# Kernel optimization log

Hardware: AMD Instinct MI355X
Metric: run time of the kernel (lower is better)

## Reference

```python
import jax, jax.numpy as jnp
import numpy as np

DIM = 3072
NHEADS = 24
HEAD_DIM = DIM // NHEADS  # 128
C = HEAD_DIM // 2         # 64 rotary pairs
B = 2
L = 2048
MAXPOS = 64
EPS = 1e-6
C1 = C - 2 * (C // 3)     # 22 (F band)
C2 = C // 3               # 21 (H band)
C3 = C // 3               # 21 (W band)


def _rope_table():
    # cos/sin table [MAXPOS, C, 2]; three independent frequency bands (F,H,W)
    pos = np.arange(MAXPOS, dtype=np.float32)
    parts = []
    for ck in (C1, C2, C3):
        inv = 1.0 / (10000.0 ** (np.arange(ck, dtype=np.float32) / ck))
        ang = np.outer(pos, inv)
        parts.append(np.stack([np.cos(ang), np.sin(ang)], axis=-1))
    return np.concatenate(parts, axis=1).astype(np.float32)


def setup_inputs() -> dict:
    key = jax.random.key(0)
    ks = jax.random.split(key, 12)
    x = jax.random.normal(ks[0], (B, L, DIM), dtype=jnp.float32)
    grid_sizes = np.array([[4, 16, 28], [4, 16, 32]], dtype=np.int32)  # ragged: 1792, 2048 tokens
    seq_lens = np.array([g[0] * g[1] * g[2] for g in grid_sizes], dtype=np.int32)
    freqs = jnp.asarray(_rope_table())
    w_scale = 0.02
    wq = jax.random.normal(ks[1], (DIM, DIM), dtype=jnp.float32) * w_scale
    wk = jax.random.normal(ks[2], (DIM, DIM), dtype=jnp.float32) * w_scale
    wv = jax.random.normal(ks[3], (DIM, DIM), dtype=jnp.float32) * w_scale
    wo = jax.random.normal(ks[4], (DIM, DIM), dtype=jnp.float32) * w_scale
    bq = jnp.zeros((DIM,), jnp.float32)
    bk = jnp.zeros((DIM,), jnp.float32)
    bv = jnp.zeros((DIM,), jnp.float32)
    bo = jnp.zeros((DIM,), jnp.float32)
    gq = jnp.ones((DIM,), jnp.float32)  # norm_q weight
    gk = jnp.ones((DIM,), jnp.float32)  # norm_k weight
    return {"x": x, "seq_lens": seq_lens, "grid_sizes": grid_sizes, "freqs": freqs,
            "wq": wq, "bq": bq, "wk": wk, "bk": bk, "wv": wv, "bv": bv,
            "wo": wo, "bo": bo, "gq": gq, "gk": gk}


def _rmsnorm(x, g):
    # WanRMSNorm: normalize in bf16, cast back, scale by bf16 weight
    xb = x.astype(jnp.bfloat16)
    n = xb * jax.lax.rsqrt(jnp.mean(xb * xb, axis=-1, keepdims=True) + jnp.bfloat16(EPS))
    return n.astype(x.dtype) * g.astype(jnp.bfloat16)


def _build_rot(grid_sizes, freqs):
    # Per-sample 3D rope rotation table [B, L, C, 2]; padded tail gets identity rotation
    gs = np.asarray(grid_sizes)
    rots = []
    for f, h, w in gs.tolist():
        s = f * h * w
        bf = jnp.broadcast_to(freqs[:f, :C1][:, None, None], (f, h, w, C1, 2))
        bh = jnp.broadcast_to(freqs[:h, C1:C1 + C2][None, :, None], (f, h, w, C2, 2))
        bw = jnp.broadcast_to(freqs[:w, C1 + C2:][None, None, :], (f, h, w, C3, 2))
        rot = jnp.concatenate([bf, bh, bw], axis=3).reshape(s, C, 2)
        if s < L:
            ident = jnp.zeros((L - s, C, 2), freqs.dtype).at[..., 0].set(1.0)
            rot = jnp.concatenate([rot, ident], axis=0)
        rots.append(rot)
    return jnp.stack(rots)


def _apply_rope(x, rot):
    # complex multiply expressed as real rotation; matches rope_apply_3d, output rounded to bf16
    xr = x.reshape(B, L, NHEADS, C, 2)
    cos = rot[:, :, None, :, 0]
    sin = rot[:, :, None, :, 1]
    out_r = xr[..., 0] * cos - xr[..., 1] * sin
    out_i = xr[..., 0] * sin + xr[..., 1] * cos
    out = jnp.stack([out_r, out_i], axis=-1).reshape(B, L, NHEADS, HEAD_DIM)
    return out.astype(jnp.bfloat16).astype(x.dtype)


def reference(x, seq_lens, grid_sizes, freqs, wq, bq, wk, bk, wv, bv, wo, bo, gq, gk):
    q = _rmsnorm(x @ wq + bq, gq).reshape(B, L, NHEADS, HEAD_DIM)
    k = _rmsnorm(x @ wk + bk, gk).reshape(B, L, NHEADS, HEAD_DIM)
    v = (x @ wv + bv).reshape(B, L, NHEADS, HEAD_DIM)
    rot = _build_rot(grid_sizes, freqs)
    q = _apply_rope(q, rot)
    k = _apply_rope(k, rot)
    scale = 1.0 / np.sqrt(HEAD_DIM).astype(np.float32)
    scores = jnp.einsum('bsnd,btnd->bnst', q, k) * scale  # [B, H, L, L]
    kmask = (jnp.arange(L)[None, :] < jnp.asarray(seq_lens)[:, None])[:, None, None, :]
    scores = jnp.where(kmask, scores, jnp.float32(-1e9))
    probs = jax.nn.softmax(scores, axis=-1)
    out = jnp.einsum('bnst,btnd->bsnd', probs, v).reshape(B, L, DIM)
    return out @ wo + bo
```

## Files before the change

### kernel.cpp

```cpp
#include <hip/hip_runtime.h>
#include <stdint.h>
#include <stddef.h>


typedef __attribute__((ext_vector_type(8))) short short8;
typedef __attribute__((ext_vector_type(4))) float f32x4;
typedef __attribute__((ext_vector_type(4))) unsigned short ushort4v;
typedef __attribute__((address_space(1))) uint32_t gu32;
typedef __attribute__((address_space(3))) uint32_t lu32;

__device__ __forceinline__ float btof(unsigned short u){
  union { float f; uint32_t i; } x; x.i = ((uint32_t)u) << 16; return x.f;
}
__device__ __forceinline__ unsigned short ftob(float f){
  uint32_t u = __builtin_bit_cast(uint32_t, f);
  u += 0x7fffu + ((u >> 16) & 1u);
  return (unsigned short)(u >> 16);
}
__device__ __forceinline__ float rb(float f){ return btof(ftob(f)); }

__device__ __forceinline__ void async_cp16(const void* g, void* l){
  __builtin_amdgcn_global_load_lds((gu32*)g, (lu32*)l, 16, 0, 0);
}

__device__ __forceinline__ void barrier_raw(){
  asm volatile("" ::: "memory");
  __builtin_amdgcn_s_barrier();
  asm volatile("" ::: "memory");
}

__device__ __forceinline__ f32x4 vmax4(f32x4 a, f32x4 b){
  f32x4 r;
  r[0] = fmaxf(a[0], b[0]); r[1] = fmaxf(a[1], b[1]);
  r[2] = fmaxf(a[2], b[2]); r[3] = fmaxf(a[3], b[3]);
  return r;
}

#define VMW4 asm volatile("s_waitcnt vmcnt(4)" ::: "memory")
#define VMW2 asm volatile("s_waitcnt vmcnt(2)" ::: "memory")
#define VMW0 asm volatile("s_waitcnt vmcnt(0)" ::: "memory")


__global__ __launch_bounds__(256) void k_convert_x(const float* __restrict__ x,
                                                   unsigned short* __restrict__ xb){
  int i = (blockIdx.x * 256 + threadIdx.x) * 4;
  float4 v = *(const float4*)(x + i);
  ushort4v o = { ftob(v.x), ftob(v.y), ftob(v.z), ftob(v.w) };
  *(ushort4v*)(xb + i) = o;
}

__global__ __launch_bounds__(256) void k_bias(const float* __restrict__ bq,
                                              const float* __restrict__ bk,
                                              const float* __restrict__ bv,
                                              float* __restrict__ bias9){
  int i = blockIdx.x * 256 + threadIdx.x;
  const float* s = (i < 3072) ? bq : ((i < 6144) ? bk : bv);
  bias9[i] = s[i % 3072];
}

__global__ __launch_bounds__(256) void k_wt(const float* __restrict__ wq,
                                            const float* __restrict__ wk,
                                            const float* __restrict__ wv,
                                            const float* __restrict__ wo,
                                            unsigned short* __restrict__ WTqkv,
                                            unsigned short* __restrict__ woT){
  __shared__ float tile[64][65];
  int k0 = blockIdx.x * 64;
  int n0g = blockIdx.y * 64;
  const float* src; unsigned short* dst; int col0, drow0;
  if (n0g < 9216){
    int sel = n0g / 3072;
    src = (sel == 0) ? wq : ((sel == 1) ? wk : wv);
    col0 = n0g % 3072; dst = WTqkv; drow0 = n0g;
  } else { src = wo; col0 = n0g - 9216; dst = woT; drow0 = n0g - 9216; }
  for (int i = 0; i < 16; i++){
    int idx = i * 256 + threadIdx.x;
    int r = idx >> 6, c = idx & 63;
    tile[r][c] = src[(size_t)(k0 + r) * 3072 + col0 + c];
  }
  __syncthreads();
  for (int i = 0; i < 16; i++){
    int idx = i * 256 + threadIdx.x;
    int rr = idx >> 6, cc = idx & 63;
    dst[(size_t)(drow0 + rr) * 3072 + k0 + cc] = ftob(tile[cc][rr]);
  }
}

template <bool OUT_BF16>
__global__ __launch_bounds__(512, 2) void k_gemm(const unsigned short* __restrict__ A,
                                                 const unsigned short* __restrict__ BT,
                                                 const float* __restrict__ bias,
                                                 void* __restrict__ Cout, int N, int K){
  extern __shared__ unsigned short lds[];
  unsigned short* AsL = lds;
  unsigned short* BsL = lds + 32768;

  int tid = threadIdx.x;
  int w = tid >> 6, lane = tid & 63;
  int quad = lane >> 4, l16 = lane & 15;
  int wr = w >> 2, wc = w & 3;
  int m0 = blockIdx.y * 256, n0 = blockIdx.x * 256;

  f32x4 acc[8][4] = {};
  short8 af[4][2], b0[2][2], b1[2][2];

  auto lda = [&](const unsigned short* base, int mh){
#pragma unroll
    for (int im = 0; im < 4; im++)
#pragma unroll
      for (int kk = 0; kk < 2; kk++){
        int j = wr * 64 + mh * 32 + im * 8 + (l16 >> 1);
        int lc = ((l16 & 1) << 3) | (kk << 2) | quad;
        af[im][kk] = *(const short8*)(base + j * 128 + (lc ^ (j & 15)) * 8);
      }
  };
  auto ldb = [&](const unsigned short* base, short8 (&bb)[2][2], int nh){
#pragma unroll
    for (int in = 0; in < 2; in++)
#pragma unroll
      for (int kk = 0; kk < 2; kk++){
        int j = wc * 32 + nh * 16 + in * 8 + (l16 >> 1);
        int lc = ((l16 & 1) << 3) | (kk << 2) | quad;
        bb[in][kk] = *(const short8*)(base + j * 128 + (lc ^ (j & 15)) * 8);
      }
  };
  auto mfmaQ = [&](int mh, short8 (&bb)[2][2], int nh){
    __builtin_amdgcn_s_setprio(1);
#pragma unroll
    for (int im = 0; im < 4; im++)
#pragma unroll
      for (int in = 0; in < 2; in++)
#pragma unroll
        for (int kk = 0; kk < 2; kk++)
          acc[mh * 4 + im][nh * 2 + in] =
            __builtin_amdgcn_mfma_f32_16x16x32_bf16(af[im][kk], bb[in][kk],
                                                    acc[mh * 4 + im][nh * 2 + in], 0, 0, 0);
    __builtin_amdgcn_s_setprio(0);
  };

  auto stageA = [&](unsigned short* dst, int kt, int mh){
#pragma unroll
    for (int i = 0; i < 2; i++){
      int idx0 = (w * 2 + i) * 8;
      int mr0 = (((idx0 >> 6) << 7) | (idx0 & 63)) | (mh << 6);
      int jb = mr0 >> 1;
      int j = jb + (lane >> 4);
      int lc = (lane & 15) ^ (j & 15);
      int mr = (j << 1) + (lc >> 3);
      async_cp16(A + (size_t)(m0 + mr) * K + kt + (lc & 7) * 8, dst + jb * 128);
    }
  };
  auto stageB = [&](unsigned short* dst, int kt, int nh){
#pragma unroll
    for (int i = 0; i < 2; i++){
      int idx0 = (w * 2 + i) * 8;
      int nr0 = (((idx0 >> 5) << 6) | (idx0 & 31)) | (nh << 5);
      int jb = nr0 >> 1;
      int j = jb + (lane >> 4);
      int lc = (lane & 15) ^ (j & 15);
      int nr = (j << 1) + (lc >> 3);
      async_cp16(BT + (size_t)(n0 + nr) * K + kt + (lc & 7) * 8, dst + jb * 128);
    }
  };

  int nt = K >> 6;
  stageA(AsL, 0, 0); stageB(BsL, 0, 0); stageB(BsL, 0, 1); stageA(AsL, 0, 1);
  VMW4; barrier_raw();

  for (int t = 0; t < nt; t++){
    unsigned short* Asb = AsL + (t & 1) * 16384;
    unsigned short* Bsb = BsL + (t & 1) * 16384;
    unsigned short* Asn = AsL + ((t & 1) ^ 1) * 16384;
    unsigned short* Bsn = BsL + ((t & 1) ^ 1) * 16384;
    int ktn = (t + 1) << 6;
    bool more = (t + 1 < nt);

    lda(Asb, 0); ldb(Bsb, b0, 0);
    if (more) stageA(Asn, ktn, 0);
    VMW4; barrier_raw();
    mfmaQ(0, b0, 0);
    barrier_raw();

    ldb(Bsb, b1, 1);
    if (more){ stageB(Bsn, ktn, 0); VMW4; } else VMW2;
    barrier_raw();
    mfmaQ(0, b1, 1);
    barrier_raw();

    lda(Asb, 1);
    if (more){ stageB(Bsn, ktn, 1); VMW4; } else VMW0;
    barrier_raw();
    mfmaQ(1, b1, 1);
    barrier_raw();

    if (more){ stageA(Asn, ktn, 1); VMW4; }
    barrier_raw();
    mfmaQ(1, b0, 0);
    barrier_raw();
  }

#pragma unroll
  for (int img = 0; img < 8; img++){
    int row = m0 + wr * 128 + img * 16 + quad * 4;
#pragma unroll
    for (int ing = 0; ing < 4; ing++){
      int col = n0 + wc * 64 + ing * 16 + l16;
      float bb = bias[col];
      f32x4 v = acc[img][ing];
#pragma unroll
      for (int r = 0; r < 4; r++){
        float out = v[r] + bb;
        if (OUT_BF16) ((unsigned short*)Cout)[(size_t)(row + r) * N + col] = ftob(out);
        else          ((float*)Cout)[(size_t)(row + r) * N + col] = out;
      }
    }
  }
}

__global__ __launch_bounds__(256) void k_rmsnorm_rope(const unsigned short* __restrict__ QKVr,
        const float* __restrict__ gq, const float* __restrict__ gk,
        const int* __restrict__ grid_sizes, const float* __restrict__ freqs,
        unsigned short* __restrict__ Qh, unsigned short* __restrict__ Kh){
  int row = blockIdx.x;
  int which = blockIdx.y;
  int b = row >> 11, s = row & 2047;
  const unsigned short* xrow = QKVr + (size_t)row * 9216 + which * 3072;
  const float* g = which ? gk : gq;
  unsigned short* out = which ? Kh : Qh;

  int tid = threadIdx.x, w = tid >> 6, lane = tid & 63;
  float ss = 0.f;
  for (int i = tid * 4; i < 3072; i += 1024){
    ushort4v v = *(const ushort4v*)(xrow + i);
    for (int j = 0; j < 4; j++){
      float f = btof(v[j]);
      ss += btof(ftob(f * f));
    }
  }
  for (int off = 32; off; off >>= 1) ss += __shfl_down(ss, off);
  __shared__ float red[4];
  if (lane == 0) red[w] = ss;
  __syncthreads();
  float tot = red[0] + red[1] + red[2] + red[3];
  float m = rb(tot * (1.0f / 3072.0f));
  m = rb(m + rb(1e-6f));
  float rn = rb(rsqrtf(m));

  int f = grid_sizes[b * 3], hh = grid_sizes[b * 3 + 1], ww = grid_sizes[b * 3 + 2];
  int fhw = f * hh * ww;

  for (int p = tid; p < 1536; p += 256){
    int c = p & 63, hd = p >> 6;
    int e0 = hd * 128 + 2 * c;
    uint32_t xp = *(const uint32_t*)(xrow + e0);
    float2 gg = *(const float2*)(g + e0);
    float x0 = rb(btof((unsigned short)(xp & 0xffffu)) * rn) * rb(gg.x);
    float x1 = rb(btof((unsigned short)(xp >> 16)) * rn) * rb(gg.y);
    float cs = 1.f, sn = 0.f;
    if (s < fhw){
      int pos;
      if (c < 22) pos = s / (hh * ww);
      else if (c < 43) pos = (s / ww) % hh;
      else pos = s % ww;
      float2 f2 = *(const float2*)(freqs + (pos * 64 + c) * 2);
      cs = f2.x; sn = f2.y;
    }
    float o0 = x0 * cs - x1 * sn;
    float o1 = x0 * sn + x1 * cs;
    size_t ob = ((size_t)((b * 24 + hd) * 2048 + s)) * 128 + 2 * c;
    uint32_t op = ((uint32_t)ftob(o1) << 16) | (uint32_t)ftob(o0);
    *(uint32_t*)(out + ob) = op;
  }
}

__global__ __launch_bounds__(256) void k_build_vt(const unsigned short* __restrict__ QKVr,
                                                  unsigned short* __restrict__ Vt){
  __shared__ unsigned short tile[64][132];
  int bh = blockIdx.x;
  int b = bh / 24, h = bh % 24;
  int t0 = blockIdx.y * 64;
  for (int i = 0; i < 8; i++){
    int idx = i * 1024 + threadIdx.x * 4;
    int r = idx >> 7, c = idx & 127;
    *(ushort4v*)&tile[r][c] =
      *(const ushort4v*)&QKVr[(size_t)(b * 2048 + t0 + r) * 9216 + 6144 + h * 128 + c];
  }
  __syncthreads();
  for (int i = 0; i < 8; i++){
    int idx = i * 1024 + threadIdx.x * 4;
    int d = idx >> 6, t = idx & 63;
    ushort4v o4 = { tile[t][d], tile[t + 1][d], tile[t + 2][d], tile[t + 3][d] };
    *(ushort4v*)&Vt[((size_t)bh * 128 + d) * 2048 + t0 + t] = o4;
  }
}

__global__ __launch_bounds__(512, 4) void k_attn(const unsigned short* __restrict__ Q,
              const unsigned short* __restrict__ Kt, const unsigned short* __restrict__ Vt,
              const int* __restrict__ seq_lens, unsigned short* __restrict__ Obuf){
  int qt = blockIdx.x, h = blockIdx.y, b = blockIdx.z;
  int bh = b * 24 + h;
  int tid = threadIdx.x, w = tid >> 6, lane = tid & 63;
  int quad = lane >> 4, l16 = lane & 15;
  int sl = seq_lens[b];
  int nkt = (sl + 63) >> 6;

  __shared__ __align__(16) unsigned short Ks[64 * 128];
  __shared__ __align__(16) unsigned short Vs[128 * 64];
  __shared__ __align__(16) unsigned short Ps[8][16 * 64];

  const unsigned short* Qb = Q + ((size_t)bh * 2048 + qt * 128 + w * 16) * 128;
  short8 qf[4];
  for (int ks = 0; ks < 4; ks++)
    qf[ks] = *(const short8*)(Qb + l16 * 128 + ks * 32 + quad * 8);

  f32x4 o[8] = {};
  float mrow = -1e30f, lrow = 0.f;

  const float ksc = 0.08838834764831845f * 1.4426950408889634f;

  const unsigned short* Kg0 = Kt + (size_t)bh * 2048 * 128;
  const unsigned short* Vg0 = Vt + (size_t)bh * 128 * 2048;

  int vrow = lane >> 3;
  int vchunk = (lane & 7) ^ (vrow & 7);

  auto stageK = [&](int t0){
    for (int i = 0; i < 2; i++){
      int rowi = w * 8 + i * 4;
      int kchunk = l16 ^ ((rowi + quad) & 15);
      async_cp16(Kg0 + (size_t)(t0 + rowi + quad) * 128 + kchunk * 8,
                 (unsigned short*)Ks + rowi * 128);
    }
  };
  auto stageV = [&](int t0){
    for (int i = 0; i < 2; i++){
      int rowi = w * 16 + i * 8;
      async_cp16(Vg0 + (size_t)(rowi + vrow) * 2048 + t0 + vchunk * 8,
                 (unsigned short*)Vs + rowi * 64);
    }
  };

  stageK(0);
  asm volatile("s_waitcnt vmcnt(0)" ::: "memory");
  barrier_raw();

  for (int kt = 0; kt < nkt; kt++){
    int t0 = kt * 64;

    stageV(t0);

    f32x4 sac[4] = {};
    for (int ks = 0; ks < 4; ks++){
      int kcs = ((ks * 4 + quad) ^ l16) * 8;
      short8 kf[4];
      for (int ct = 0; ct < 4; ct++)
        kf[ct] = *(const short8*)(Ks + (ct * 16 + l16) * 128 + kcs);
      __builtin_amdgcn_s_setprio(1);
      for (int ct = 0; ct < 4; ct++)
        sac[ct] = __builtin_amdgcn_mfma_f32_16x16x32_bf16(kf[ct], qf[ks], sac[ct], 0, 0, 0);
      __builtin_amdgcn_s_setprio(0);
    }

    asm volatile("s_waitcnt lgkmcnt(0)" ::: "memory");
    barrier_raw();

    bool haveK = (kt + 1 < nkt);
    if (haveK) stageK(t0 + 64);

    if (t0 + 64 > sl){
      for (int ct = 0; ct < 4; ct++)
        for (int r = 0; r < 4; r++)
          if (t0 + ct * 16 + quad * 4 + r >= sl) sac[ct][r] = -1e30f;
    }

    {
      f32x4 m03 = vmax4(vmax4(sac[0], sac[1]), vmax4(sac[2], sac[3]));
      float mx = fmaxf(fmaxf(m03[0], m03[1]), fmaxf(m03[2], m03[3]));
      mx = fmaxf(mx, __shfl_xor(mx, 16));
      mx = fmaxf(mx, __shfl_xor(mx, 32));
      float mnew = mrow;
      if (!__all((mx - mrow) * ksc <= 11.5f)){
        mnew = fmaxf(mrow, mx);
        float alpha = exp2f((mrow - mnew) * ksc);
        mrow = mnew;
        lrow *= alpha;
        for (int r = 0; r < 4; r++){
          float ar = __shfl(alpha, quad * 4 + r, 16);
          for (int dt = 0; dt < 8; dt++) o[dt][r] *= ar;
        }
      }
      float psum = 0.f;
      for (int ct = 0; ct < 4; ct++){
        ushort4v pw;
        for (int r = 0; r < 4; r++){
          float p = exp2f((sac[ct][r] - mnew) * ksc);
          unsigned short pb = ftob(p);
          psum += btof(pb);
          pw[r] = pb;
        }
        int cpos = (ct * 2 + (quad >> 1)) ^ (l16 & 7);
        *(ushort4v*)&Ps[w][l16 * 64 + cpos * 8 + (quad & 1) * 4] = pw;
      }
      psum += __shfl_xor(psum, 16);
      psum += __shfl_xor(psum, 32);
      lrow += psum;
    }

    if (haveK) asm volatile("s_waitcnt vmcnt(2)" ::: "memory");
    else       asm volatile("s_waitcnt vmcnt(0)" ::: "memory");
    barrier_raw();

    asm volatile("s_waitcnt lgkmcnt(0)" ::: "memory");

    for (int ks = 0; ks < 2; ks++){
      int vcs = ((ks * 4 + quad) ^ (l16 & 7)) * 8;
      short8 pf = *(const short8*)(&Ps[w][l16 * 64 + vcs]);
      for (int dh = 0; dh < 2; dh++){
        short8 vf[4];
        for (int dt = 0; dt < 4; dt++)
          vf[dt] = *(const short8*)(Vs + ((dh * 4 + dt) * 16 + l16) * 64 + vcs);
        __builtin_amdgcn_s_setprio(1);
        for (int dt = 0; dt < 4; dt++)
          o[dh * 4 + dt] = __builtin_amdgcn_mfma_f32_16x16x32_bf16(pf, vf[dt], o[dh * 4 + dt], 0, 0, 0);
        __builtin_amdgcn_s_setprio(0);
      }
    }

    asm volatile("s_waitcnt lgkmcnt(0)" ::: "memory");
    asm volatile("s_waitcnt vmcnt(0)" ::: "memory");
    barrier_raw();
  }

  float inv = 1.0f / lrow;
  for (int r = 0; r < 4; r++){
    float invr = __shfl(inv, quad * 4 + r, 16);
    int s = qt * 128 + w * 16 + quad * 4 + r;
    size_t base = (size_t)(b * 2048 + s) * 3072 + h * 128;
    for (int dt = 0; dt < 8; dt++)
      Obuf[base + dt * 16 + l16] = ftob(o[dt][r] * invr);
  }
}


extern "C" void kernel_launch(void* const* d_in, const int* in_sizes, int n_in,
                              void* d_out, int out_size, void* d_ws, size_t ws_size,
                              hipStream_t stream){
  const float* x          = (const float*)d_in[0];
  const int*   seq_lens   = (const int*)d_in[1];
  const int*   grid_sizes = (const int*)d_in[2];
  const float* freqs      = (const float*)d_in[3];
  const float* wq = (const float*)d_in[4];
  const float* bq = (const float*)d_in[5];
  const float* wk = (const float*)d_in[6];
  const float* bk = (const float*)d_in[7];
  const float* wv = (const float*)d_in[8];
  const float* bv = (const float*)d_in[9];
  const float* wo = (const float*)d_in[10];
  const float* bo = (const float*)d_in[11];
  const float* gq = (const float*)d_in[12];
  const float* gk = (const float*)d_in[13];

  char* ws = (char*)d_ws;
  unsigned short* Xb    = (unsigned short*)(ws);
  unsigned short* WTqkv = (unsigned short*)(ws + 25165824);
  unsigned short* woT   = (unsigned short*)(ws + 81788928);
  float*          bias9 = (float*)(ws + 100663296);
  unsigned short* QKVr  = (unsigned short*)(ws + 100700160);
  unsigned short* Qh    = (unsigned short*)(ws + 176197632);
  unsigned short* Kh    = (unsigned short*)(ws + 201363456);
  unsigned short* Vth   = (unsigned short*)(ws + 226529280);
  unsigned short* Obuf  = Xb;

  static bool s_attr = false;
  if (!s_attr){
    hipFuncSetAttribute(reinterpret_cast<const void*>(&k_gemm<true>),
                        hipFuncAttributeMaxDynamicSharedMemorySize, 131072);
    hipFuncSetAttribute(reinterpret_cast<const void*>(&k_gemm<false>),
                        hipFuncAttributeMaxDynamicSharedMemorySize, 131072);
    s_attr = true;
  }

  k_convert_x<<<12288, 256, 0, stream>>>(x, Xb);
  k_bias<<<36, 256, 0, stream>>>(bq, bk, bv, bias9);
  k_wt<<<dim3(48, 192), 256, 0, stream>>>(wq, wk, wv, wo, WTqkv, woT);
  k_gemm<true><<<dim3(36, 16), 512, 131072, stream>>>(Xb, WTqkv, bias9, QKVr, 9216, 3072);
  k_rmsnorm_rope<<<dim3(4096, 2), 256, 0, stream>>>(QKVr, gq, gk, grid_sizes, freqs, Qh, Kh);
  k_build_vt<<<dim3(48, 32), 256, 0, stream>>>(QKVr, Vth);
  k_attn<<<dim3(16, 24, 2), 512, 0, stream>>>(Qh, Kh, Vth, seq_lens, Obuf);
  k_gemm<false><<<dim3(12, 16), 512, 131072, stream>>>(Obuf, woT, bo, (float*)d_out, 3072, 3072);
}
```

Before: 748.3 us.

## Deepen GEMM prefetch pipeline and halve barriers per k-tile

Restructures the double-buffered GEMM main loop so quarter-tiles for k-step t+2 are staged into the current buffer as soon as the matching fragments have been read out of it. Each iteration now uses four barriers instead of eight, and the vmcnt waits allow up to six loads in flight. The goal is more load/compute overlap and less synchronisation stall. The trade-off is more fragile ordering of LDS reuse, where a wrong wait count or a buffer hazard would corrupt results.

```diff
diff --git a/kernel.cpp b/kernel.cpp
--- a/kernel.cpp
+++ b/kernel.cpp
@@ -36,6 +36,7 @@
   return r;
 }
 
+#define VMW6 asm volatile("s_waitcnt vmcnt(6)" ::: "memory")
 #define VMW4 asm volatile("s_waitcnt vmcnt(4)" ::: "memory")
 #define VMW2 asm volatile("s_waitcnt vmcnt(2)" ::: "memory")
 #define VMW0 asm volatile("s_waitcnt vmcnt(0)" ::: "memory")
@@ -164,39 +165,42 @@
   };
 
   int nt = K >> 6;
-  stageA(AsL, 0, 0); stageB(BsL, 0, 0); stageB(BsL, 0, 1); stageA(AsL, 0, 1);
-  VMW4; barrier_raw();
+  unsigned short* Abuf[2] = { AsL, AsL + 16384 };
+  unsigned short* Bbuf[2] = { BsL, BsL + 16384 };
+
+  stageA(Abuf[0], 0, 0);  stageB(Bbuf[0], 0, 0);
+  stageB(Bbuf[0], 0, 1);  stageA(Abuf[0], 0, 1);
+  stageA(Abuf[1], 64, 0); stageB(Bbuf[1], 64, 0);
+  VMW6; barrier_raw();
 
   for (int t = 0; t < nt; t++){
-    unsigned short* Asb = AsL + (t & 1) * 16384;
-    unsigned short* Bsb = BsL + (t & 1) * 16384;
-    unsigned short* Asn = AsL + ((t & 1) ^ 1) * 16384;
-    unsigned short* Bsn = BsL + ((t & 1) ^ 1) * 16384;
-    int ktn = (t + 1) << 6;
-    bool more = (t + 1 < nt);
-
-    lda(Asb, 0); ldb(Bsb, b0, 0);
-    if (more) stageA(Asn, ktn, 0);
-    VMW4; barrier_raw();
+    unsigned short* Ab = Abuf[t & 1];
+    unsigned short* Bb = Bbuf[t & 1];
+    unsigned short* An = Abuf[(t & 1) ^ 1];
+    unsigned short* Bn = Bbuf[(t & 1) ^ 1];
+    bool s1 = (t + 1 < nt), s2 = (t + 2 < nt);
+
+    lda(Ab, 0); ldb(Bb, b0, 0);
+    if (s1) stageB(Bn, (t + 1) << 6, 1);
+    if (t == nt - 1) VMW2;
+    barrier_raw();
     mfmaQ(0, b0, 0);
-    barrier_raw();
-
-    ldb(Bsb, b1, 1);
-    if (more){ stageB(Bsn, ktn, 0); VMW4; } else VMW2;
+
+    ldb(Bb, b1, 1);
+    if (s1) stageA(An, (t + 1) << 6, 1);
+    if (t == nt - 1) VMW0; else VMW6;
     barrier_raw();
     mfmaQ(0, b1, 1);
-    barrier_raw();
-
-    lda(Asb, 1);
-    if (more){ stageB(Bsn, ktn, 1); VMW4; } else VMW0;
+
+    lda(Ab, 1);
+    if (s2) stageA(Ab, (t + 2) << 6, 0);
     barrier_raw();
     mfmaQ(1, b1, 1);
-    barrier_raw();
-
-    if (more){ stageA(Asn, ktn, 1); VMW4; }
+
+    if (s2) stageB(Bb, (t + 2) << 6, 0);
+    if (t <= nt - 3) VMW6; else if (t == nt - 2) VMW4;
     barrier_raw();
     mfmaQ(1, b0, 0);
-    barrier_raw();
   }
 
 #pragma unroll
```

Result: slower. 981.3 us (+31.1%).
